# Optimization experiments

Measured on AMD Instinct MI355X. Metric: run time of the kernel, lower is better.

## Reference

```python
import jax, jax.numpy as jnp
from jax import lax
import numpy as np

B, D, L = 32, 64, 4096
E = 8          # num_experts
K = 2          # top-k
OC = 32        # out_channels


def setup_inputs() -> dict:
    key = jax.random.key(0)
    ks = jax.random.split(key, 6)
    x = jax.random.normal(ks[0], (B, D, L), dtype=jnp.float32)
    # gating weight [D*5, E] (torch init is zeros; use small random for a meaningful reference)
    w_gate = jax.random.normal(ks[1], (D * 5, E), dtype=jnp.float32) * 0.02
    # Conv1d(D -> OC, kernel 3)
    conv1_w = jax.random.normal(ks[2], (OC, D, 3), dtype=jnp.float32) * (1.0 / np.sqrt(D * 3))
    conv1_b = jax.random.normal(ks[3], (OC,), dtype=jnp.float32) * 0.01
    # Conv1d(OC -> OC*E, kernel 1)
    conv2_w = jax.random.normal(ks[4], (OC * E, OC, 1), dtype=jnp.float32) * (1.0 / np.sqrt(OC))
    conv2_b = jax.random.normal(ks[5], (OC * E,), dtype=jnp.float32) * 0.01
    return {"x": x, "w_gate": w_gate, "conv1_w": conv1_w, "conv1_b": conv1_b,
            "conv2_w": conv2_w, "conv2_b": conv2_b}


def _gates(g_in, w_gate):
    # eval-mode noisy_top_k_gating: no noise, softmax -> top-(k+1) -> renormalize top-k -> scatter
    logits = jax.nn.softmax(g_in @ w_gate, axis=1)            # [B, E]
    top_v, top_i = lax.top_k(logits, min(K + 1, E))           # sorted descending
    vk = top_v[:, :K]
    ik = top_i[:, :K]
    gk = vk / (jnp.sum(vk, axis=1, keepdims=True) + 1e-6)
    gates = jnp.zeros_like(logits).at[jnp.arange(logits.shape[0])[:, None], ik].set(gk)
    return gates


def reference(x, w_gate, conv1_w, conv1_b, conv2_w, conv2_b):
    b, d, l = x.shape
    g_in = x[:, :, -6:-1].reshape(b, d * 5)                   # last-5-timestep gating features
    gates = _gates(g_in, w_gate)                              # [B, E]
    dn = ("NCH", "OIH", "NCH")
    h = lax.conv_general_dilated(x, conv1_w, (1,), "VALID", dimension_numbers=dn)
    h = jnp.tanh(h + conv1_b[None, :, None])                  # [B, OC, L-2]
    out = lax.conv_general_dilated(h, conv2_w, (1,), "VALID", dimension_numbers=dn)
    out = out + conv2_b[None, :, None]                        # [B, OC*E, L']
    lp = out.shape[-1]
    out = out.transpose(0, 2, 1).reshape(b, lp, OC, E)        # [B, L', OC, E]
    moe = jnp.einsum("blde,be->bld", out, gates)              # weighted combine
    return moe.transpose(0, 2, 1)                             # [B, OC, L']
```

## Files before the change

### kernel.cpp

```cpp
#include <hip/hip_runtime.h>
#include <math.h>

#define B_  32
#define D_  64
#define L_  4096
#define E_  8
#define OC_ 32
#define LP_ 4094
#define TILE 64
#define NT   64

typedef __attribute__((ext_vector_type(8)))  short short8;
typedef __attribute__((ext_vector_type(16))) float float16;

static __device__ __forceinline__ unsigned short f2bf(float f) {
    unsigned u = __float_as_uint(f);
    return (unsigned short)((u + 0x7fffu + ((u >> 16) & 1u)) >> 16);
}
static __device__ __forceinline__ unsigned cvtpk(float a, float b) {
    unsigned r;
    asm("v_cvt_pk_bf16_f32 %0, %1, %2" : "=v"(r) : "v"(a), "v"(b));
    return r;
}
static __device__ __forceinline__ float fast_tanh(float x) {
    float e = __expf(2.0f * x);
    return fmaf(-2.0f, __builtin_amdgcn_rcpf(e + 1.0f), 1.0f);
}


__global__ __launch_bounds__(256)
void prep_kernel(const float* __restrict__ x,
                 const float* __restrict__ w_gate,
                 const float* __restrict__ c1w,
                 const float* __restrict__ c2w,
                 const float* __restrict__ c2b,
                 float* __restrict__ beff,
                 unsigned short* __restrict__ aF,
                 unsigned short* __restrict__ wf2)
{
    const int tid = threadIdx.x;

    if (blockIdx.x == 8) {
        for (int i = tid; i < 12 * 64 * 8; i += 256) {
            int ks = i >> 9, lane = (i >> 3) & 63, ii = i & 7;
            int oc = lane & 31, half = lane >> 5;
            int kp = ks * 16 + half * 8 + ii;
            int t = kp >> 6, c = kp & 63;
            aF[i] = f2bf(c1w[oc * 192 + c * 3 + t]);
        }
        return;
    }

    const int wv = tid >> 6, lane = tid & 63;
    const int b  = blockIdx.x * 4 + wv;
    const int d  = lane;

    float xv[5];
    #pragma unroll
    for (int t = 0; t < 5; ++t)
        xv[t] = x[((size_t)b * D_ + d) * L_ + (L_ - 6) + t];

    float part[E_];
    #pragma unroll
    for (int e = 0; e < E_; ++e) part[e] = 0.f;
    #pragma unroll
    for (int t = 0; t < 5; ++t) {
        const float* wg = w_gate + (d * 5 + t) * E_;
        #pragma unroll
        for (int e = 0; e < E_; ++e) part[e] += xv[t] * wg[e];
    }
    #pragma unroll
    for (int off = 1; off < 64; off <<= 1) {
        #pragma unroll
        for (int e = 0; e < E_; ++e)
            part[e] += __shfl_xor(part[e], off, 64);
    }
    float m = part[0];
    #pragma unroll
    for (int e = 1; e < E_; ++e) m = fmaxf(m, part[e]);
    float p[E_], s = 0.f;
    #pragma unroll
    for (int e = 0; e < E_; ++e) { p[e] = expf(part[e] - m); s += p[e]; }
    float inv = 1.f / s;
    #pragma unroll
    for (int e = 0; e < E_; ++e) p[e] *= inv;

    int i0 = 0;
    #pragma unroll
    for (int e = 1; e < E_; ++e) if (p[e] > p[i0]) i0 = e;
    int i1 = (i0 == 0) ? 1 : 0;
    #pragma unroll
    for (int e = 0; e < E_; ++e) {
        if (e == i0) continue;
        if (p[e] > p[i1]) i1 = e;
    }
    const float v0 = p[i0], v1 = p[i1];
    const float den = v0 + v1 + 1e-6f;
    const float g0 = v0 / den, g1 = v1 / den;

    {
        const int dd = lane & 31, half = lane >> 5;
        #pragma unroll
        for (int ks = 0; ks < 2; ++ks) {
            #pragma unroll
            for (int i = 0; i < 8; ++i) {
                int oc = ks * 16 + half * 8 + i;
                float v = g0 * c2w[(dd * E_ + i0) * OC_ + oc]
                        + g1 * c2w[(dd * E_ + i1) * OC_ + oc];
                wf2[((b * 2 + ks) * 64 + lane) * 8 + i] = f2bf(v);
            }
        }
    }
    if (d < OC_)
        beff[b * OC_ + d] = g0 * c2b[d * E_ + i0] + g1 * c2b[d * E_ + i1];
}

__global__ __launch_bounds__(128, 4)
void fused_main(const float* __restrict__ x,
                const unsigned short* __restrict__ aF,
                const unsigned short* __restrict__ wf2,
                const float* __restrict__ beff,
                const float* __restrict__ c1b,
                float* __restrict__ out)
{
    __shared__ __align__(16) unsigned short xT[66 * 64];

    const int tid  = threadIdx.x;
    const int lane = tid & 63;
    const int wv   = tid >> 6;
    const int b    = blockIdx.x >> 6;
    const int l0   = (blockIdx.x & 63) << 6;
    const float* xb = x + (size_t)b * (D_ * L_);

    {
        const int c2 = tid >> 2;
        const int j4 = (tid & 3) << 2;
        const float* p0 = xb + (size_t)(2 * c2) * L_ + l0;
        const float* p1 = p0 + L_;
        #pragma unroll
        for (int jq = 0; jq < 4; ++jq) {
            int j = jq * 16 + j4;
            float4 v0 = *(const float4*)(p0 + j);
            float4 v1 = *(const float4*)(p1 + j);
            float e0[4] = {v0.x, v0.y, v0.z, v0.w};
            float e1[4] = {v1.x, v1.y, v1.z, v1.w};
            #pragma unroll
            for (int r = 0; r < 4; ++r) {
                int row = j + r;
                int off = (row * 128 + c2 * 4) ^ ((row & 7) << 4);
                *(unsigned*)((char*)xT + off) = cvtpk(e0[r], e1[r]);
            }
        }
        if (tid < 64) {
            int cc2 = tid >> 1, jj = tid & 1;
            int row = TILE + jj;
            int lg  = l0 + row;
            float f0 = 0.f, f1 = 0.f;
            if (lg < L_) {
                f0 = xb[(size_t)(2 * cc2) * L_ + lg];
                f1 = xb[(size_t)(2 * cc2 + 1) * L_ + lg];
            }
            int off = (row * 128 + cc2 * 4) ^ ((row & 7) << 4);
            *(unsigned*)((char*)xT + off) = cvtpk(f0, f1);
        }
    }

    short8 a1[12];
    #pragma unroll
    for (int ks = 0; ks < 12; ++ks)
        a1[ks] = *(const short8*)(aF + (ks * 64 + lane) * 8);

    const int cl = lane & 31;
    const int hi = lane >> 5;

    __syncthreads();

    const int cb = wv * 32;
    float16 acc = (float16)0.0f;
    #pragma unroll
    for (int t = 0; t < 3; ++t) {
        int row = cb + cl + t;
        int rb  = row * 128;
        int swz = (row & 7) << 4;
        #pragma unroll
        for (int q = 0; q < 4; ++q) {
            int off = (rb + q * 32 + hi * 16) ^ swz;
            short8 bf = *(const short8*)((const char*)xT + off);
            acc = __builtin_amdgcn_mfma_f32_32x32x16_bf16(a1[t * 4 + q], bf, acc, 0, 0, 0);
        }
    }

    short8 a2[2];
    a2[0] = *(const short8*)(wf2 + ((b * 2 + 0) * 64 + lane) * 8);
    a2[1] = *(const short8*)(wf2 + ((b * 2 + 1) * 64 + lane) * 8);

    float th[16];
    #pragma unroll
    for (int r = 0; r < 16; ++r) {
        int row = (r & 3) + 8 * (r >> 2) + 4 * hi;
        th[r] = fast_tanh(acc[r] + c1b[row]);
    }

    unsigned x0a = hi ? cvtpk(th[0],  th[1])  : cvtpk(th[4],  th[5]);
    unsigned x0b = hi ? cvtpk(th[2],  th[3])  : cvtpk(th[6],  th[7]);
    unsigned x1a = hi ? cvtpk(th[8],  th[9])  : cvtpk(th[12], th[13]);
    unsigned x1b = hi ? cvtpk(th[10], th[11]) : cvtpk(th[14], th[15]);
    unsigned r0a = (unsigned)__shfl_xor((int)x0a, 32, 64);
    unsigned r0b = (unsigned)__shfl_xor((int)x0b, 32, 64);
    unsigned r1a = (unsigned)__shfl_xor((int)x1a, 32, 64);
    unsigned r1b = (unsigned)__shfl_xor((int)x1b, 32, 64);

    union U { short8 s8; unsigned u[4]; };
    U b0, b1;
    b0.u[0] = hi ? r0a : cvtpk(th[0], th[1]);
    b0.u[1] = hi ? r0b : cvtpk(th[2], th[3]);
    b0.u[2] = hi ? cvtpk(th[4], th[5]) : r0a;
    b0.u[3] = hi ? cvtpk(th[6], th[7]) : r0b;
    b1.u[0] = hi ? r1a : cvtpk(th[8], th[9]);
    b1.u[1] = hi ? r1b : cvtpk(th[10], th[11]);
    b1.u[2] = hi ? cvtpk(th[12], th[13]) : r1a;
    b1.u[3] = hi ? cvtpk(th[14], th[15]) : r1b;

    float16 acc2 = (float16)0.0f;
    acc2 = __builtin_amdgcn_mfma_f32_32x32x16_bf16(a2[0], b0.s8, acc2, 0, 0, 0);
    acc2 = __builtin_amdgcn_mfma_f32_32x32x16_bf16(a2[1], b1.s8, acc2, 0, 0, 0);

    int l = l0 + cb + cl;
    if (l < LP_) {
        const float* be = beff + b * OC_;
        float* ob = out + (size_t)b * (OC_ * (size_t)LP_) + l;
        #pragma unroll
        for (int r = 0; r < 16; ++r) {
            int row = (r & 3) + 8 * (r >> 2) + 4 * hi;
            ob[(size_t)row * LP_] = acc2[r] + be[row];
        }
    }
}

extern "C" void kernel_launch(void* const* d_in, const int* in_sizes, int n_in,
                              void* d_out, int out_size, void* d_ws, size_t ws_size,
                              hipStream_t stream)
{
    const float* x      = (const float*)d_in[0];
    const float* w_gate = (const float*)d_in[1];
    const float* c1w    = (const float*)d_in[2];
    const float* c1b    = (const float*)d_in[3];
    const float* c2w    = (const float*)d_in[4];
    const float* c2b    = (const float*)d_in[5];
    float* out = (float*)d_out;

    char* ws = (char*)d_ws;
    float* beff         = (float*)ws;
    unsigned short* aF  = (unsigned short*)(ws + 4096);
    unsigned short* wf2 = (unsigned short*)(ws + 16384);

    prep_kernel<<<9, 256, 0, stream>>>(x, w_gate, c1w, c2w, c2b, beff, aF, wf2);
    fused_main<<<B_ * NT, 128, 0, stream>>>(x, aF, wf2, beff, c1b, out);
}
```

Measured before the change: 22.83 us.

## Use larger 512-thread blocks with two-stage register prefetch of input tiles

Replaces 2048 small 128-thread blocks, each handling 64 positions, with 256 blocks of 512 threads that each process 512 positions as two 256-wide tiles. The second tile's global loads are issued into registers before the first tile is computed, so load latency overlaps the MFMA work. Weight fragments are loaded once per block instead of once per 64 positions. In exchange it uses larger LDS buffers and more registers, and 256 blocks may underfill the GPU's compute units.

```diff
diff --git a/kernel.cpp b/kernel.cpp
--- a/kernel.cpp
+++ b/kernel.cpp
@@ -7,8 +7,6 @@
 #define E_  8
 #define OC_ 32
 #define LP_ 4094
-#define TILE 64
-#define NT   64
 
 typedef __attribute__((ext_vector_type(8)))  short short8;
 typedef __attribute__((ext_vector_type(16))) float float16;
@@ -26,7 +24,6 @@
     float e = __expf(2.0f * x);
     return fmaf(-2.0f, __builtin_amdgcn_rcpf(e + 1.0f), 1.0f);
 }
-
 
 __global__ __launch_bounds__(256)
 void prep_kernel(const float* __restrict__ x,
@@ -115,66 +112,14 @@
         beff[b * OC_ + d] = g0 * c2b[d * E_ + i0] + g1 * c2b[d * E_ + i1];
 }
 
-__global__ __launch_bounds__(128, 4)
-void fused_main(const float* __restrict__ x,
-                const unsigned short* __restrict__ aF,
-                const unsigned short* __restrict__ wf2,
-                const float* __restrict__ beff,
-                const float* __restrict__ c1b,
-                float* __restrict__ out)
+static __device__ __forceinline__ void compute_tile(
+    const unsigned short* __restrict__ xbuf,
+    const short8* a1, const short8* a2,
+    const float* __restrict__ c1b,
+    const float* __restrict__ be,
+    float* __restrict__ outb,
+    int l0, int wv, int cl, int hi)
 {
-    __shared__ __align__(16) unsigned short xT[66 * 64];
-
-    const int tid  = threadIdx.x;
-    const int lane = tid & 63;
-    const int wv   = tid >> 6;
-    const int b    = blockIdx.x >> 6;
-    const int l0   = (blockIdx.x & 63) << 6;
-    const float* xb = x + (size_t)b * (D_ * L_);
-
-    {
-        const int c2 = tid >> 2;
-        const int j4 = (tid & 3) << 2;
-        const float* p0 = xb + (size_t)(2 * c2) * L_ + l0;
-        const float* p1 = p0 + L_;
-        #pragma unroll
-        for (int jq = 0; jq < 4; ++jq) {
-            int j = jq * 16 + j4;
-            float4 v0 = *(const float4*)(p0 + j);
-            float4 v1 = *(const float4*)(p1 + j);
-            float e0[4] = {v0.x, v0.y, v0.z, v0.w};
-            float e1[4] = {v1.x, v1.y, v1.z, v1.w};
-            #pragma unroll
-            for (int r = 0; r < 4; ++r) {
-                int row = j + r;
-                int off = (row * 128 + c2 * 4) ^ ((row & 7) << 4);
-                *(unsigned*)((char*)xT + off) = cvtpk(e0[r], e1[r]);
-            }
-        }
-        if (tid < 64) {
-            int cc2 = tid >> 1, jj = tid & 1;
-            int row = TILE + jj;
-            int lg  = l0 + row;
-            float f0 = 0.f, f1 = 0.f;
-            if (lg < L_) {
-                f0 = xb[(size_t)(2 * cc2) * L_ + lg];
-                f1 = xb[(size_t)(2 * cc2 + 1) * L_ + lg];
-            }
-            int off = (row * 128 + cc2 * 4) ^ ((row & 7) << 4);
-            *(unsigned*)((char*)xT + off) = cvtpk(f0, f1);
-        }
-    }
-
-    short8 a1[12];
-    #pragma unroll
-    for (int ks = 0; ks < 12; ++ks)
-        a1[ks] = *(const short8*)(aF + (ks * 64 + lane) * 8);
-
-    const int cl = lane & 31;
-    const int hi = lane >> 5;
-
-    __syncthreads();
-
     const int cb = wv * 32;
     float16 acc = (float16)0.0f;
     #pragma unroll
@@ -185,14 +130,10 @@
         #pragma unroll
         for (int q = 0; q < 4; ++q) {
             int off = (rb + q * 32 + hi * 16) ^ swz;
-            short8 bf = *(const short8*)((const char*)xT + off);
+            short8 bf = *(const short8*)((const char*)xbuf + off);
             acc = __builtin_amdgcn_mfma_f32_32x32x16_bf16(a1[t * 4 + q], bf, acc, 0, 0, 0);
         }
     }
-
-    short8 a2[2];
-    a2[0] = *(const short8*)(wf2 + ((b * 2 + 0) * 64 + lane) * 8);
-    a2[1] = *(const short8*)(wf2 + ((b * 2 + 1) * 64 + lane) * 8);
 
     float th[16];
     #pragma unroll
@@ -227,14 +168,125 @@
 
     int l = l0 + cb + cl;
     if (l < LP_) {
-        const float* be = beff + b * OC_;
-        float* ob = out + (size_t)b * (OC_ * (size_t)LP_) + l;
+        float* ob = outb + l;
         #pragma unroll
         for (int r = 0; r < 16; ++r) {
             int row = (r & 3) + 8 * (r >> 2) + 4 * hi;
             ob[(size_t)row * LP_] = acc2[r] + be[row];
         }
     }
+}
+
+__global__ __launch_bounds__(512, 2)
+void fused_main(const float* __restrict__ x,
+                const unsigned short* __restrict__ aF,
+                const unsigned short* __restrict__ wf2,
+                const float* __restrict__ beff,
+                const float* __restrict__ c1b,
+                float* __restrict__ out)
+{
+    __shared__ __align__(16) unsigned short xT0[260 * 64];
+    __shared__ __align__(16) unsigned short xT1[260 * 64];
+
+    const int tid  = threadIdx.x;
+    const int lane = tid & 63;
+    const int wv   = tid >> 6;
+    const int b    = blockIdx.x >> 3;
+    const int S    = (blockIdx.x & 7) << 9;
+    const float* xb = x + (size_t)b * (D_ * L_);
+
+    const int c2 = tid >> 4;
+    const int jb = (tid & 15) << 2;
+    const float* p0 = xb + (size_t)(2 * c2) * L_;
+    const float* p1 = p0 + L_;
+    const int haloc = tid >> 1;
+    const int haloj = tid & 1;
+
+    float4 A0[4], A1[4];
+    #pragma unroll
+    for (int jq = 0; jq < 4; ++jq) {
+        int j = S + jq * 64 + jb;
+        A0[jq] = *(const float4*)(p0 + j);
+        A1[jq] = *(const float4*)(p1 + j);
+    }
+    float hA0 = 0.f, hA1 = 0.f;
+    if (tid < 64) {
+        int lg = S + 256 + haloj;
+        hA0 = xb[(size_t)(2 * haloc) * L_ + lg];
+        hA1 = xb[(size_t)(2 * haloc + 1) * L_ + lg];
+    }
+
+    short8 a1[12];
+    #pragma unroll
+    for (int ks = 0; ks < 12; ++ks)
+        a1[ks] = *(const short8*)(aF + (ks * 64 + lane) * 8);
+    short8 a2[2];
+    a2[0] = *(const short8*)(wf2 + ((b * 2 + 0) * 64 + lane) * 8);
+    a2[1] = *(const short8*)(wf2 + ((b * 2 + 1) * 64 + lane) * 8);
+    const float* be = beff + b * OC_;
+    float* outb = out + (size_t)b * (OC_ * (size_t)LP_);
+
+    const int cl = lane & 31;
+    const int hi = lane >> 5;
+
+    #pragma unroll
+    for (int jq = 0; jq < 4; ++jq) {
+        float e0[4] = {A0[jq].x, A0[jq].y, A0[jq].z, A0[jq].w};
+        float e1[4] = {A1[jq].x, A1[jq].y, A1[jq].z, A1[jq].w};
+        #pragma unroll
+        for (int r = 0; r < 4; ++r) {
+            int row = jq * 64 + jb + r;
+            int off = (row * 128 + c2 * 4) ^ ((row & 7) << 4);
+            *(unsigned*)((char*)xT0 + off) = cvtpk(e0[r], e1[r]);
+        }
+    }
+    if (tid < 64) {
+        int row = 256 + haloj;
+        int off = (row * 128 + haloc * 4) ^ ((row & 7) << 4);
+        *(unsigned*)((char*)xT0 + off) = cvtpk(hA0, hA1);
+    }
+
+    float4 B0[4], B1[4];
+    #pragma unroll
+    for (int jq = 0; jq < 4; ++jq) {
+        int j = S + 256 + jq * 64 + jb;
+        B0[jq] = *(const float4*)(p0 + j);
+        B1[jq] = *(const float4*)(p1 + j);
+    }
+    float hB0 = 0.f, hB1 = 0.f;
+    if (tid < 64) {
+        int lg = S + 512 + haloj;
+        if (lg > L_ - 1) lg = L_ - 1;
+        hB0 = xb[(size_t)(2 * haloc) * L_ + lg];
+        hB1 = xb[(size_t)(2 * haloc + 1) * L_ + lg];
+    }
+
+    __syncthreads();
+
+    compute_tile(xT0, a1, a2, c1b, be, outb, S, wv, cl, hi);
+
+    __syncthreads();
+
+    #pragma unroll
+    for (int jq = 0; jq < 4; ++jq) {
+        float e0[4] = {B0[jq].x, B0[jq].y, B0[jq].z, B0[jq].w};
+        float e1[4] = {B1[jq].x, B1[jq].y, B1[jq].z, B1[jq].w};
+        #pragma unroll
+        for (int r = 0; r < 4; ++r) {
+            int row = jq * 64 + jb + r;
+            int off = (row * 128 + c2 * 4) ^ ((row & 7) << 4);
+            *(unsigned*)((char*)xT1 + off) = cvtpk(e0[r], e1[r]);
+        }
+    }
+    if (tid < 64) {
+        int row = 256 + haloj;
+        int off = (row * 128 + haloc * 4) ^ ((row & 7) << 4);
+        *(unsigned*)((char*)xT1 + off) = cvtpk(hB0, hB1);
+    }
+
+    __syncthreads();
+
+    compute_tile(xT1, a1, a2, c1b, be, outb, S + 256, wv, cl, hi);
 }
 
 extern "C" void kernel_launch(void* const* d_in, const int* in_sizes, int n_in,
@@ -255,5 +307,5 @@
     unsigned short* wf2 = (unsigned short*)(ws + 16384);
 
     prep_kernel<<<9, 256, 0, stream>>>(x, w_gate, c1w, c2w, c2b, beff, aF, wf2);
-    fused_main<<<B_ * NT, 128, 0, stream>>>(x, aF, wf2, beff, c1b, out);
-}
+    fused_main<<<B_ * 8, 512, 0, stream>>>(x, aF, wf2, beff, c1b, out);
+}
```

Measured after the change: 22.75 us. About the same (-0.3%).
